# Kernel tuning notes

Hardware: AMD Instinct MI355X
Metric: run time of the kernel (lower is better)

The kernel has to match this reference:

```python
import jax, jax.numpy as jnp
import numpy as np

N_REF, N_IN, D_FEAT, P, N_ELEM = 4096, 8192, 512, 256, 4


def setup_inputs() -> dict:
    key = jax.random.key(0)
    k1, k2, k3, k4, k5 = jax.random.split(key, 5)
    return {
        "Alpha": jax.random.normal(k1, (P, N_REF), dtype=jnp.float32) * 0.05,
        "X_ref": jax.random.normal(k2, (N_REF, D_FEAT), dtype=jnp.float32),
        "desc": jax.random.normal(k3, (N_IN, D_FEAT), dtype=jnp.float32),
        "Z_ref": jax.random.randint(k4, (N_REF,), 0, N_ELEM, dtype=jnp.int32),
        "Z": jax.random.randint(k5, (N_IN,), 0, N_ELEM, dtype=jnp.int32),
        "expK": 2,
    }


def reference(Alpha, X_ref, desc, Z_ref, Z, expK):
    # Per-element grouped kernel: K[i, j] = (X_ref[i] . desc[j])**expK,
    # contribution only where ref atom i and query atom j share the element.
    # This is exactly the gather -> per-element GEMM+pow -> combine -> scatter
    # of the original module, expressed as one masked dense computation.
    K = jnp.power(jnp.matmul(X_ref, desc.T), expK)          # [N_ref, N_in]
    same_elem = Z_ref[:, None] == Z[None, :]                # [N_ref, N_in]
    K_masked = jnp.where(same_elem, K, jnp.zeros((), K.dtype))
    y = jnp.matmul(Alpha, K_masked)                          # [P, N_in]
    return y
```

## Files before the change

kernel.cpp:

```cpp
#include <hip/hip_runtime.h>
#include <stdint.h>

#define P_DIM 256
#define NREF  4096
#define NIN   8192
#define DF    512
#define NE    4
#define CREF  1536
#define CIN   2560
#define AE_LD (NE * CREF)

typedef __bf16 bf16x8 __attribute__((ext_vector_type(8)));
typedef float  f32x4  __attribute__((ext_vector_type(4)));
typedef unsigned short ush8 __attribute__((ext_vector_type(8)));

static __device__ __forceinline__ unsigned short f2bf(float f) {
    uint32_t u = __builtin_bit_cast(uint32_t, f);
    u += 0x7FFFu + ((u >> 16) & 1u);
    return (unsigned short)(u >> 16);
}

__global__ __launch_bounds__(256) void plan_sort(
    const int* __restrict__ Zr, const int* __restrict__ Z,
    int* __restrict__ iperm, int* __restrict__ jperm, int* __restrict__ cnt) {
    __shared__ int histX[NE][256];
    __shared__ int histD[NE][256];
    const int t = threadIdx.x;
    constexpr int CHX = NREF / 256;
    constexpr int CHD = NIN / 256;

    int lc[NE];
#pragma unroll
    for (int e = 0; e < NE; ++e) lc[e] = 0;
    for (int k = 0; k < CHX; ++k) lc[Zr[t * CHX + k] & (NE - 1)]++;
#pragma unroll
    for (int e = 0; e < NE; ++e) histX[e][t] = lc[e];

#pragma unroll
    for (int e = 0; e < NE; ++e) lc[e] = 0;
    for (int k = 0; k < CHD; ++k) lc[Z[t * CHD + k] & (NE - 1)]++;
#pragma unroll
    for (int e = 0; e < NE; ++e) histD[e][t] = lc[e];

    __syncthreads();
    if (t < 2 * NE) {
        int b = t & (NE - 1);
        int isD = t >> 2;
        int run = 0;
        if (!isD) {
            for (int u = 0; u < 256; ++u) { int v = histX[b][u]; histX[b][u] = run; run += v; }
            cnt[b] = run;
        } else {
            for (int u = 0; u < 256; ++u) { int v = histD[b][u]; histD[b][u] = run; run += v; }
            cnt[NE + b] = run;
        }
    }
    __syncthreads();

    int off[NE];
#pragma unroll
    for (int e = 0; e < NE; ++e) off[e] = histX[e][t];
    for (int k = 0; k < CHX; ++k) {
        int i = t * CHX + k;
        int e = Zr[i] & (NE - 1);
        iperm[e * CREF + off[e]++] = i;
    }
#pragma unroll
    for (int e = 0; e < NE; ++e) off[e] = histD[e][t];
    for (int k = 0; k < CHD; ++k) {
        int j = t * CHD + k;
        int e = Z[j] & (NE - 1);
        jperm[e * CIN + off[e]++] = j;
    }
}

#define GATHER_BLOCKS (NE * (CREF + CIN) / 4)
#define ALPHA_BLOCKS  (P_DIM * AE_LD / (256 * 8))

__global__ void gather_all(const float* __restrict__ Alpha,
                           const float* __restrict__ X_ref, const float* __restrict__ desc,
                           const int* __restrict__ iperm, const int* __restrict__ jperm,
                           const int* __restrict__ cnt,
                           unsigned short* __restrict__ Xe, unsigned short* __restrict__ De,
                           unsigned short* __restrict__ Ae) {
    if (blockIdx.x < GATHER_BLOCKS) {
        int w = (blockIdx.x * blockDim.x + threadIdx.x) >> 6;
        int lane = threadIdx.x & 63;
        const float* src = nullptr;
        unsigned short* dstp;
        if (w < NE * CREF) {
            int e = w / CREF, s = w - e * CREF;
            if (s < cnt[e]) src = X_ref + (size_t)iperm[w] * DF;
            dstp = Xe + (size_t)w * DF;
        } else {
            int w2 = w - NE * CREF;
            int e = w2 / CIN, s = w2 - e * CIN;
            if (s < cnt[NE + e]) src = desc + (size_t)jperm[w2] * DF;
            dstp = De + (size_t)w2 * DF;
        }
        ush8 o;
        if (src) {
            float4 a = *(const float4*)(src + lane * 8);
            float4 b = *(const float4*)(src + lane * 8 + 4);
            o[0] = f2bf(a.x); o[1] = f2bf(a.y); o[2] = f2bf(a.z); o[3] = f2bf(a.w);
            o[4] = f2bf(b.x); o[5] = f2bf(b.y); o[6] = f2bf(b.z); o[7] = f2bf(b.w);
        } else {
            o = (ush8){0, 0, 0, 0, 0, 0, 0, 0};
        }
        *(ush8*)(dstp + lane * 8) = o;
    } else {
        int idx8 = (blockIdx.x - GATHER_BLOCKS) * 256 + threadIdx.x;
        int p = idx8 / (AE_LD / 8);
        int c8 = idx8 - p * (AE_LD / 8);
        int col0 = c8 * 8;
        int e = col0 / CREF;
        int ic0 = col0 - e * CREF;
        int cn = cnt[e];
        const int* ip = iperm + col0;
        ush8 v;
#pragma unroll
        for (int k = 0; k < 8; ++k) {
            unsigned short r = 0;
            if (ic0 + k < cn) r = f2bf(Alpha[(size_t)p * NREF + ip[k]]);
            v[k] = r;
        }
        *(ush8*)(Ae + (size_t)idx8 * 8) = v;
    }
}

__global__ __launch_bounds__(256) void g1_grouped(
    const unsigned short* __restrict__ DeA, const unsigned short* __restrict__ XeA,
    unsigned short* __restrict__ KtA, const int* __restrict__ cnt) {
    constexpr int BK = 64;
    const int e = blockIdx.z;
    const int padR = (cnt[e] + 127) & ~127;
    const int padI = (cnt[NE + e] + 127) & ~127;
    const int m0 = blockIdx.y * 128;
    const int n0 = blockIdx.x * 128;
    if (m0 >= padI || n0 >= padR) return;

    const unsigned short* A = DeA + (size_t)e * CIN * DF;
    const unsigned short* B = XeA + (size_t)e * CREF * DF;
    unsigned short* C = KtA + (size_t)e * CIN * CREF;

    __shared__ unsigned short tA[128 * BK];
    __shared__ unsigned short tB[128 * BK];

    const int tid = threadIdx.x, wave = tid >> 6, lane = tid & 63;
    const int wr = wave >> 1, wc = wave & 1;
    const int waveM = wr * 64, waveN = wc * 64;
    const int lrow = lane >> 3, ls = lane & 7;
    const int l15 = lane & 15, lq = lane >> 4;

    f32x4 acc[4][4];
#pragma unroll
    for (int r = 0; r < 4; ++r)
#pragma unroll
        for (int c = 0; c < 4; ++c) acc[r][c] = (f32x4){0.f, 0.f, 0.f, 0.f};

#pragma unroll 1
    for (int k0 = 0; k0 < DF; k0 += BK) {
        __syncthreads();
#pragma unroll
        for (int it = 0; it < 8; ++it) {
            int cb = wave + it * 4;
            bool isB = cb >= 16;
            int cb2 = isB ? cb - 16 : cb;
            int row = cb2 * 8 + lrow;
            int g = ls ^ (row & 7);
            const unsigned short* gp = (isB ? B : A)
                + (size_t)((isB ? n0 : m0) + row) * DF + (size_t)(k0 + g * 8);
            unsigned short* lp = (isB ? tB : tA) + cb2 * (8 * BK);
            __builtin_amdgcn_global_load_lds(
                (const __attribute__((address_space(1))) void*)gp,
                (__attribute__((address_space(3))) void*)lp, 16, 0, 0);
        }
        __syncthreads();
#pragma unroll
        for (int kk = 0; kk < BK; kk += 32) {
            const int cbase = kk >> 3;
            bf16x8 af[4], bfr[4];
#pragma unroll
            for (int r = 0; r < 4; ++r) {
                int m = waveM + r * 16 + l15;
                int ch = (cbase + lq) ^ (m & 7);
                af[r] = *(const bf16x8*)&tA[m * BK + ch * 8];
            }
#pragma unroll
            for (int c = 0; c < 4; ++c) {
                int n = waveN + c * 16 + l15;
                int ch = (cbase + lq) ^ (n & 7);
                bfr[c] = *(const bf16x8*)&tB[n * BK + ch * 8];
            }
#pragma unroll
            for (int r = 0; r < 4; ++r)
#pragma unroll
                for (int c = 0; c < 4; ++c)
                    acc[r][c] = __builtin_amdgcn_mfma_f32_16x16x32_bf16(
                        af[r], bfr[c], acc[r][c], 0, 0, 0);
        }
    }

#pragma unroll
    for (int r = 0; r < 4; ++r) {
        int mb = m0 + waveM + r * 16 + lq * 4;
#pragma unroll
        for (int reg = 0; reg < 4; ++reg) {
            size_t ro = (size_t)(mb + reg) * CREF;
#pragma unroll
            for (int c = 0; c < 4; ++c) {
                int n = n0 + waveN + c * 16 + l15;
                float v = acc[r][c][reg];
                C[ro + n] = f2bf(v * v);
            }
        }
    }
}

__global__ __launch_bounds__(256) void g2_grouped(
    const unsigned short* __restrict__ Ae, const unsigned short* __restrict__ KtA,
    const int* __restrict__ jperm, const int* __restrict__ cnt,
    float* __restrict__ out) {
    constexpr int BK = 64;
    const int e = blockIdx.z;
    const int cntI = cnt[NE + e];
    const int padR = (cnt[e] + 127) & ~127;
    const int n0 = blockIdx.x * 64;
    const int m0 = blockIdx.y * 128;
    if (n0 >= cntI) return;

    const unsigned short* B = KtA + (size_t)e * CIN * CREF;

    __shared__ unsigned short tA[2][128 * BK];
    __shared__ unsigned short tB[2][64 * BK];

    const int tid = threadIdx.x, wave = tid >> 6, lane = tid & 63;
    const int wr = wave >> 1, wc = wave & 1;
    const int waveM = wr * 64, waveN = wc * 32;
    const int lrow = lane >> 3, ls = lane & 7;
    const int l15 = lane & 15, lq = lane >> 4;

    auto stage = [&](int buf, int k0) {
#pragma unroll
        for (int it = 0; it < 6; ++it) {
            int cb = wave + it * 4;
            bool isB = cb >= 16;
            int cb2 = isB ? cb - 16 : cb;
            int row = cb2 * 8 + lrow;
            int g = ls ^ (row & 7);
            const unsigned short* gp = isB
                ? B + (size_t)(n0 + row) * CREF + (size_t)(k0 + g * 8)
                : Ae + (size_t)(m0 + row) * AE_LD + (size_t)(e * CREF + k0 + g * 8);
            unsigned short* lp = (isB ? tB[buf] : tA[buf]) + cb2 * (8 * BK);
            __builtin_amdgcn_global_load_lds(
                (const __attribute__((address_space(1))) void*)gp,
                (__attribute__((address_space(3))) void*)lp, 16, 0, 0);
        }
    };

    f32x4 acc[4][2];
#pragma unroll
    for (int r = 0; r < 4; ++r)
#pragma unroll
        for (int c = 0; c < 2; ++c) acc[r][c] = (f32x4){0.f, 0.f, 0.f, 0.f};

    if (padR > 0) {
        stage(0, 0);
        __syncthreads();
        int buf = 0;
#pragma unroll 1
        for (int k0 = 0; k0 < padR; k0 += BK) {
            if (k0 + BK < padR) stage(buf ^ 1, k0 + BK);
#pragma unroll
            for (int kk = 0; kk < BK; kk += 32) {
                const int cbase = kk >> 3;
                bf16x8 af[4], bfr[2];
#pragma unroll
                for (int r = 0; r < 4; ++r) {
                    int m = waveM + r * 16 + l15;
                    int ch = (cbase + lq) ^ (m & 7);
                    af[r] = *(const bf16x8*)&tA[buf][m * BK + ch * 8];
                }
#pragma unroll
                for (int c = 0; c < 2; ++c) {
                    int n = waveN + c * 16 + l15;
                    int ch = (cbase + lq) ^ (n & 7);
                    bfr[c] = *(const bf16x8*)&tB[buf][n * BK + ch * 8];
                }
#pragma unroll
                for (int r = 0; r < 4; ++r)
#pragma unroll
                    for (int c = 0; c < 2; ++c)
                        acc[r][c] = __builtin_amdgcn_mfma_f32_16x16x32_bf16(
                            af[r], bfr[c], acc[r][c], 0, 0, 0);
            }
            __syncthreads();
            buf ^= 1;
        }
    }

    int jok[2], jdest[2];
#pragma unroll
    for (int c = 0; c < 2; ++c) {
        int jl = n0 + waveN + c * 16 + l15;
        jok[c] = jl < cntI;
        jdest[c] = jok[c] ? jperm[e * CIN + jl] : 0;
    }
#pragma unroll
    for (int r = 0; r < 4; ++r) {
        int pb = m0 + waveM + r * 16 + lq * 4;
#pragma unroll
        for (int reg = 0; reg < 4; ++reg) {
            size_t ro = (size_t)(pb + reg) * NIN;
#pragma unroll
            for (int c = 0; c < 2; ++c)
                if (jok[c]) out[ro + jdest[c]] = acc[r][c][reg];
        }
    }
}

extern "C" void kernel_launch(void* const* d_in, const int* in_sizes, int n_in,
                              void* d_out, int out_size, void* d_ws, size_t ws_size,
                              hipStream_t stream) {
    const float* Alpha = (const float*)d_in[0];
    const float* X_ref = (const float*)d_in[1];
    const float* desc  = (const float*)d_in[2];
    const int*   Z_ref = (const int*)d_in[3];
    const int*   Z     = (const int*)d_in[4];
    float* out = (float*)d_out;

    unsigned short* Xe = (unsigned short*)d_ws;
    unsigned short* De = Xe + (size_t)NE * CREF * DF;
    unsigned short* Ae = De + (size_t)NE * CIN * DF;
    unsigned short* Kt = Ae + (size_t)P_DIM * AE_LD;
    int* iperm = (int*)(Kt + (size_t)NE * CIN * CREF);
    int* jperm = iperm + NE * CREF;
    int* cnt   = jperm + NE * CIN;

    plan_sort<<<1, 256, 0, stream>>>(Z_ref, Z, iperm, jperm, cnt);

    gather_all<<<GATHER_BLOCKS + ALPHA_BLOCKS, 256, 0, stream>>>(
        Alpha, X_ref, desc, iperm, jperm, cnt, Xe, De, Ae);

    g1_grouped<<<dim3(CREF / 128, CIN / 128, NE), 256, 0, stream>>>(De, Xe, Kt, cnt);

    g2_grouped<<<dim3(CIN / 64, P_DIM / 128, NE), 256, 0, stream>>>(Ae, Kt, jperm, cnt, out);
}
```

Baseline: 150.9 us.

## Fuse gather and both grouped GEMMs into one persistent kernel with grid barriers

After: 387.8 us. +156.9%, slower.

```diff
diff --git a/kernel.cpp b/kernel.cpp
--- a/kernel.cpp
+++ b/kernel.cpp
@@ -9,6 +9,7 @@
 #define CREF  1536
 #define CIN   2560
 #define AE_LD (NE * CREF)
+#define NBLK  512
 
 typedef __bf16 bf16x8 __attribute__((ext_vector_type(8)));
 typedef float  f32x4  __attribute__((ext_vector_type(4)));
@@ -20,14 +21,28 @@
     return (unsigned short)(u >> 16);
 }
 
+static __device__ __forceinline__ void gridbar(int* b) {
+    __syncthreads();
+    if (threadIdx.x == 0) {
+        __threadfence();
+        __hip_atomic_fetch_add(b, 1, __ATOMIC_ACQ_REL, __HIP_MEMORY_SCOPE_AGENT);
+        while (__hip_atomic_load(b, __ATOMIC_ACQUIRE, __HIP_MEMORY_SCOPE_AGENT) < NBLK)
+            __builtin_amdgcn_s_sleep(2);
+    }
+    __syncthreads();
+}
+
 __global__ __launch_bounds__(256) void plan_sort(
     const int* __restrict__ Zr, const int* __restrict__ Z,
-    int* __restrict__ iperm, int* __restrict__ jperm, int* __restrict__ cnt) {
+    int* __restrict__ iperm, int* __restrict__ jperm, int* __restrict__ cnt,
+    int* __restrict__ bar) {
     __shared__ int histX[NE][256];
     __shared__ int histD[NE][256];
     const int t = threadIdx.x;
     constexpr int CHX = NREF / 256;
     constexpr int CHD = NIN / 256;
+
+    if (t < 2) bar[t] = 0;
 
     int lc[NE];
 #pragma unroll
@@ -77,244 +92,252 @@
 #define GATHER_BLOCKS (NE * (CREF + CIN) / 4)
 #define ALPHA_BLOCKS  (P_DIM * AE_LD / (256 * 8))
 
-__global__ void gather_all(const float* __restrict__ Alpha,
-                           const float* __restrict__ X_ref, const float* __restrict__ desc,
-                           const int* __restrict__ iperm, const int* __restrict__ jperm,
-                           const int* __restrict__ cnt,
-                           unsigned short* __restrict__ Xe, unsigned short* __restrict__ De,
-                           unsigned short* __restrict__ Ae) {
-    if (blockIdx.x < GATHER_BLOCKS) {
-        int w = (blockIdx.x * blockDim.x + threadIdx.x) >> 6;
-        int lane = threadIdx.x & 63;
-        const float* src = nullptr;
-        unsigned short* dstp;
-        if (w < NE * CREF) {
-            int e = w / CREF, s = w - e * CREF;
-            if (s < cnt[e]) src = X_ref + (size_t)iperm[w] * DF;
-            dstp = Xe + (size_t)w * DF;
-        } else {
-            int w2 = w - NE * CREF;
-            int e = w2 / CIN, s = w2 - e * CIN;
-            if (s < cnt[NE + e]) src = desc + (size_t)jperm[w2] * DF;
-            dstp = De + (size_t)w2 * DF;
-        }
-        ush8 o;
-        if (src) {
-            float4 a = *(const float4*)(src + lane * 8);
-            float4 b = *(const float4*)(src + lane * 8 + 4);
-            o[0] = f2bf(a.x); o[1] = f2bf(a.y); o[2] = f2bf(a.z); o[3] = f2bf(a.w);
-            o[4] = f2bf(b.x); o[5] = f2bf(b.y); o[6] = f2bf(b.z); o[7] = f2bf(b.w);
-        } else {
-            o = (ush8){0, 0, 0, 0, 0, 0, 0, 0};
-        }
-        *(ush8*)(dstp + lane * 8) = o;
-    } else {
-        int idx8 = (blockIdx.x - GATHER_BLOCKS) * 256 + threadIdx.x;
-        int p = idx8 / (AE_LD / 8);
-        int c8 = idx8 - p * (AE_LD / 8);
-        int col0 = c8 * 8;
-        int e = col0 / CREF;
-        int ic0 = col0 - e * CREF;
-        int cn = cnt[e];
-        const int* ip = iperm + col0;
-        ush8 v;
-#pragma unroll
-        for (int k = 0; k < 8; ++k) {
-            unsigned short r = 0;
-            if (ic0 + k < cn) r = f2bf(Alpha[(size_t)p * NREF + ip[k]]);
-            v[k] = r;
-        }
-        *(ush8*)(Ae + (size_t)idx8 * 8) = v;
-    }
-}
-
-__global__ __launch_bounds__(256) void g1_grouped(
-    const unsigned short* __restrict__ DeA, const unsigned short* __restrict__ XeA,
-    unsigned short* __restrict__ KtA, const int* __restrict__ cnt) {
+__global__ __launch_bounds__(256, 2) void fused_all(
+    const float* __restrict__ Alpha, const float* __restrict__ X_ref,
+    const float* __restrict__ desc,
+    const int* __restrict__ iperm, const int* __restrict__ jperm,
+    const int* __restrict__ cnt,
+    unsigned short* __restrict__ Xe, unsigned short* __restrict__ De,
+    unsigned short* __restrict__ Ae, unsigned short* __restrict__ KtA,
+    float* __restrict__ out, int* __restrict__ bar) {
     constexpr int BK = 64;
-    const int e = blockIdx.z;
-    const int padR = (cnt[e] + 127) & ~127;
-    const int padI = (cnt[NE + e] + 127) & ~127;
-    const int m0 = blockIdx.y * 128;
-    const int n0 = blockIdx.x * 128;
-    if (m0 >= padI || n0 >= padR) return;
-
-    const unsigned short* A = DeA + (size_t)e * CIN * DF;
-    const unsigned short* B = XeA + (size_t)e * CREF * DF;
-    unsigned short* C = KtA + (size_t)e * CIN * CREF;
-
-    __shared__ unsigned short tA[128 * BK];
-    __shared__ unsigned short tB[128 * BK];
+    __shared__ unsigned short lds[24576];
 
     const int tid = threadIdx.x, wave = tid >> 6, lane = tid & 63;
     const int wr = wave >> 1, wc = wave & 1;
-    const int waveM = wr * 64, waveN = wc * 64;
     const int lrow = lane >> 3, ls = lane & 7;
     const int l15 = lane & 15, lq = lane >> 4;
 
-    f32x4 acc[4][4];
-#pragma unroll
-    for (int r = 0; r < 4; ++r)
-#pragma unroll
-        for (int c = 0; c < 4; ++c) acc[r][c] = (f32x4){0.f, 0.f, 0.f, 0.f};
-
-#pragma unroll 1
-    for (int k0 = 0; k0 < DF; k0 += BK) {
-        __syncthreads();
-#pragma unroll
-        for (int it = 0; it < 8; ++it) {
-            int cb = wave + it * 4;
-            bool isB = cb >= 16;
-            int cb2 = isB ? cb - 16 : cb;
-            int row = cb2 * 8 + lrow;
-            int g = ls ^ (row & 7);
-            const unsigned short* gp = (isB ? B : A)
-                + (size_t)((isB ? n0 : m0) + row) * DF + (size_t)(k0 + g * 8);
-            unsigned short* lp = (isB ? tB : tA) + cb2 * (8 * BK);
-            __builtin_amdgcn_global_load_lds(
-                (const __attribute__((address_space(1))) void*)gp,
-                (__attribute__((address_space(3))) void*)lp, 16, 0, 0);
+#pragma unroll 1
+    for (int vb = blockIdx.x; vb < GATHER_BLOCKS + ALPHA_BLOCKS; vb += NBLK) {
+        if (vb < GATHER_BLOCKS) {
+            int w = (vb * 256 + tid) >> 6;
+            const float* src = nullptr;
+            unsigned short* dstp;
+            if (w < NE * CREF) {
+                int e = w / CREF, s = w - e * CREF;
+                if (s < cnt[e]) src = X_ref + (size_t)iperm[w] * DF;
+                dstp = Xe + (size_t)w * DF;
+            } else {
+                int w2 = w - NE * CREF;
+                int e = w2 / CIN, s = w2 - e * CIN;
+                if (s < cnt[NE + e]) src = desc + (size_t)jperm[w2] * DF;
+                dstp = De + (size_t)w2 * DF;
+            }
+            ush8 o;
+            if (src) {
+                float4 a = *(const float4*)(src + lane * 8);
+                float4 b = *(const float4*)(src + lane * 8 + 4);
+                o[0] = f2bf(a.x); o[1] = f2bf(a.y); o[2] = f2bf(a.z); o[3] = f2bf(a.w);
+                o[4] = f2bf(b.x); o[5] = f2bf(b.y); o[6] = f2bf(b.z); o[7] = f2bf(b.w);
+            } else {
+                o = (ush8){0, 0, 0, 0, 0, 0, 0, 0};
+            }
+            *(ush8*)(dstp + lane * 8) = o;
+        } else {
+            int idx8 = (vb - GATHER_BLOCKS) * 256 + tid;
+            int p = idx8 / (AE_LD / 8);
+            int c8 = idx8 - p * (AE_LD / 8);
+            int col0 = c8 * 8;
+            int e = col0 / CREF;
+            int ic0 = col0 - e * CREF;
+            int cn = cnt[e];
+            const int* ip = iperm + col0;
+            ush8 v;
+#pragma unroll
+            for (int k = 0; k < 8; ++k) {
+                unsigned short r = 0;
+                if (ic0 + k < cn) r = f2bf(Alpha[(size_t)p * NREF + ip[k]]);
+                v[k] = r;
+            }
+            *(ush8*)(Ae + (size_t)idx8 * 8) = v;
         }
-        __syncthreads();
-#pragma unroll
-        for (int kk = 0; kk < BK; kk += 32) {
-            const int cbase = kk >> 3;
-            bf16x8 af[4], bfr[4];
+    }
+
+    gridbar(bar + 0);
+
+    {
+        unsigned short* tA = lds;
+        unsigned short* tB = lds + 8192;
+#pragma unroll 1
+        for (int vt = blockIdx.x; vt < (CREF / 128) * (CIN / 128) * NE; vt += NBLK) {
+            const int bx = vt % (CREF / 128);
+            const int rem = vt / (CREF / 128);
+            const int by = rem % (CIN / 128);
+            const int e = rem / (CIN / 128);
+            const int padR = (cnt[e] + 127) & ~127;
+            const int padI = (cnt[NE + e] + 127) & ~127;
+            const int m0 = by * 128;
+            const int n0 = bx * 128;
+            if (m0 >= padI || n0 >= padR) continue;
+
+            const unsigned short* A = De + (size_t)e * CIN * DF;
+            const unsigned short* B = Xe + (size_t)e * CREF * DF;
+            unsigned short* C = KtA + (size_t)e * CIN * CREF;
+
+            f32x4 acc[4][4];
+#pragma unroll
+            for (int r = 0; r < 4; ++r)
+#pragma unroll
+                for (int c = 0; c < 4; ++c) acc[r][c] = (f32x4){0.f, 0.f, 0.f, 0.f};
+
+            const int waveM = wr * 64, waveN = wc * 64;
+#pragma unroll 1
+            for (int k0 = 0; k0 < DF; k0 += BK) {
+                __syncthreads();
+#pragma unroll
+                for (int it = 0; it < 8; ++it) {
+                    int cb = wave + it * 4;
+                    bool isB = cb >= 16;
+                    int cb2 = isB ? cb - 16 : cb;
+                    int row = cb2 * 8 + lrow;
+                    int g = ls ^ (row & 7);
+                    const unsigned short* gp = (isB ? B : A)
+                        + (size_t)((isB ? n0 : m0) + row) * DF + (size_t)(k0 + g * 8);
+                    unsigned short* lp = (isB ? tB : tA) + cb2 * (8 * BK);
+                    __builtin_amdgcn_global_load_lds(
+                        (const __attribute__((address_space(1))) void*)gp,
+                        (__attribute__((address_space(3))) void*)lp, 16, 0, 0);
+                }
+                __syncthreads();
+#pragma unroll
+                for (int kk = 0; kk < BK; kk += 32) {
+                    const int cbase = kk >> 3;
+                    bf16x8 af[4], bfr[4];
+#pragma unroll
+                    for (int r = 0; r < 4; ++r) {
+                        int m = waveM + r * 16 + l15;
+                        int ch = (cbase + lq) ^ (m & 7);
+                        af[r] = *(const bf16x8*)&tA[m * BK + ch * 8];
+                    }
+#pragma unroll
+                    for (int c = 0; c < 4; ++c) {
+                        int n = waveN + c * 16 + l15;
+                        int ch = (cbase + lq) ^ (n & 7);
+                        bfr[c] = *(const bf16x8*)&tB[n * BK + ch * 8];
+                    }
+#pragma unroll
+                    for (int r = 0; r < 4; ++r)
+#pragma unroll
+                        for (int c = 0; c < 4; ++c)
+                            acc[r][c] = __builtin_amdgcn_mfma_f32_16x16x32_bf16(
+                                af[r], bfr[c], acc[r][c], 0, 0, 0);
+                }
+            }
+
 #pragma unroll
             for (int r = 0; r < 4; ++r) {
-                int m = waveM + r * 16 + l15;
-                int ch = (cbase + lq) ^ (m & 7);
-                af[r] = *(const bf16x8*)&tA[m * BK + ch * 8];
-            }
-#pragma unroll
-            for (int c = 0; c < 4; ++c) {
-                int n = waveN + c * 16 + l15;
-                int ch = (cbase + lq) ^ (n & 7);
-                bfr[c] = *(const bf16x8*)&tB[n * BK + ch * 8];
-            }
+                int mb = m0 + waveM + r * 16 + lq * 4;
+#pragma unroll
+                for (int reg = 0; reg < 4; ++reg) {
+                    size_t ro = (size_t)(mb + reg) * CREF;
+#pragma unroll
+                    for (int c = 0; c < 4; ++c) {
+                        int n = n0 + waveN + c * 16 + l15;
+                        float v = acc[r][c][reg];
+                        C[ro + n] = f2bf(v * v);
+                    }
+                }
+            }
+        }
+    }
+
+    gridbar(bar + 1);
+
+    {
+        unsigned short* tA2 = lds;
+        unsigned short* tB2 = lds + 16384;
+#pragma unroll 1
+        for (int vt = blockIdx.x; vt < (CIN / 64) * (P_DIM / 128) * NE; vt += NBLK) {
+            const int bx = vt % (CIN / 64);
+            const int rem = vt / (CIN / 64);
+            const int by = rem % (P_DIM / 128);
+            const int e = rem / (P_DIM / 128);
+            const int cntI = cnt[NE + e];
+            const int padR = (cnt[e] + 127) & ~127;
+            const int n0 = bx * 64;
+            const int m0 = by * 128;
+            if (n0 >= cntI) continue;
+
+            const unsigned short* B = KtA + (size_t)e * CIN * CREF;
+            const int waveM = wr * 64, waveN = wc * 32;
+
+            auto stage = [&](int buf, int k0) {
+#pragma unroll
+                for (int it = 0; it < 6; ++it) {
+                    int cb = wave + it * 4;
+                    bool isB = cb >= 16;
+                    int cb2 = isB ? cb - 16 : cb;
+                    int row = cb2 * 8 + lrow;
+                    int g = ls ^ (row & 7);
+                    const unsigned short* gp = isB
+                        ? B + (size_t)(n0 + row) * CREF + (size_t)(k0 + g * 8)
+                        : Ae + (size_t)(m0 + row) * AE_LD + (size_t)(e * CREF + k0 + g * 8);
+                    unsigned short* lp = (isB ? tB2 + buf * 4096 : tA2 + buf * 8192)
+                        + cb2 * (8 * BK);
+                    __builtin_amdgcn_global_load_lds(
+                        (const __attribute__((address_space(1))) void*)gp,
+                        (__attribute__((address_space(3))) void*)lp, 16, 0, 0);
+                }
+            };
+
+            f32x4 acc[4][2];
 #pragma unroll
             for (int r = 0; r < 4; ++r)
 #pragma unroll
-                for (int c = 0; c < 4; ++c)
-                    acc[r][c] = __builtin_amdgcn_mfma_f32_16x16x32_bf16(
-                        af[r], bfr[c], acc[r][c], 0, 0, 0);
-        }
-    }
-
-#pragma unroll
-    for (int r = 0; r < 4; ++r) {
-        int mb = m0 + waveM + r * 16 + lq * 4;
-#pragma unroll
-        for (int reg = 0; reg < 4; ++reg) {
-            size_t ro = (size_t)(mb + reg) * CREF;
-#pragma unroll
-            for (int c = 0; c < 4; ++c) {
-                int n = n0 + waveN + c * 16 + l15;
-                float v = acc[r][c][reg];
-                C[ro + n] = f2bf(v * v);
-            }
-        }
-    }
-}
-
-__global__ __launch_bounds__(256) void g2_grouped(
-    const unsigned short* __restrict__ Ae, const unsigned short* __restrict__ KtA,
-    const int* __restrict__ jperm, const int* __restrict__ cnt,
-    float* __restrict__ out) {
-    constexpr int BK = 64;
-    const int e = blockIdx.z;
-    const int cntI = cnt[NE + e];
-    const int padR = (cnt[e] + 127) & ~127;
-    const int n0 = blockIdx.x * 64;
-    const int m0 = blockIdx.y * 128;
-    if (n0 >= cntI) return;
-
-    const unsigned short* B = KtA + (size_t)e * CIN * CREF;
-
-    __shared__ unsigned short tA[2][128 * BK];
-    __shared__ unsigned short tB[2][64 * BK];
-
-    const int tid = threadIdx.x, wave = tid >> 6, lane = tid & 63;
-    const int wr = wave >> 1, wc = wave & 1;
-    const int waveM = wr * 64, waveN = wc * 32;
-    const int lrow = lane >> 3, ls = lane & 7;
-    const int l15 = lane & 15, lq = lane >> 4;
-
-    auto stage = [&](int buf, int k0) {
-#pragma unroll
-        for (int it = 0; it < 6; ++it) {
-            int cb = wave + it * 4;
-            bool isB = cb >= 16;
-            int cb2 = isB ? cb - 16 : cb;
-            int row = cb2 * 8 + lrow;
-            int g = ls ^ (row & 7);
-            const unsigned short* gp = isB
-                ? B + (size_t)(n0 + row) * CREF + (size_t)(k0 + g * 8)
-                : Ae + (size_t)(m0 + row) * AE_LD + (size_t)(e * CREF + k0 + g * 8);
-            unsigned short* lp = (isB ? tB[buf] : tA[buf]) + cb2 * (8 * BK);
-            __builtin_amdgcn_global_load_lds(
-                (const __attribute__((address_space(1))) void*)gp,
-                (__attribute__((address_space(3))) void*)lp, 16, 0, 0);
-        }
-    };
-
-    f32x4 acc[4][2];
-#pragma unroll
-    for (int r = 0; r < 4; ++r)
-#pragma unroll
-        for (int c = 0; c < 2; ++c) acc[r][c] = (f32x4){0.f, 0.f, 0.f, 0.f};
-
-    if (padR > 0) {
-        stage(0, 0);
-        __syncthreads();
-        int buf = 0;
-#pragma unroll 1
-        for (int k0 = 0; k0 < padR; k0 += BK) {
-            if (k0 + BK < padR) stage(buf ^ 1, k0 + BK);
-#pragma unroll
-            for (int kk = 0; kk < BK; kk += 32) {
-                const int cbase = kk >> 3;
-                bf16x8 af[4], bfr[2];
-#pragma unroll
-                for (int r = 0; r < 4; ++r) {
-                    int m = waveM + r * 16 + l15;
-                    int ch = (cbase + lq) ^ (m & 7);
-                    af[r] = *(const bf16x8*)&tA[buf][m * BK + ch * 8];
-                }
-#pragma unroll
-                for (int c = 0; c < 2; ++c) {
-                    int n = waveN + c * 16 + l15;
-                    int ch = (cbase + lq) ^ (n & 7);
-                    bfr[c] = *(const bf16x8*)&tB[buf][n * BK + ch * 8];
-                }
-#pragma unroll
-                for (int r = 0; r < 4; ++r)
+                for (int c = 0; c < 2; ++c) acc[r][c] = (f32x4){0.f, 0.f, 0.f, 0.f};
+
+            stage(0, 0);
+            __syncthreads();
+            int buf = 0;
+#pragma unroll 1
+            for (int k0 = 0; k0 < padR; k0 += BK) {
+                if (k0 + BK < padR) stage(buf ^ 1, k0 + BK);
+#pragma unroll
+                for (int kk = 0; kk < BK; kk += 32) {
+                    const int cbase = kk >> 3;
+                    bf16x8 af[4], bfr[2];
+#pragma unroll
+                    for (int r = 0; r < 4; ++r) {
+                        int m = waveM + r * 16 + l15;
+                        int ch = (cbase + lq) ^ (m & 7);
+                        af[r] = *(const bf16x8*)&tA2[buf * 8192 + m * BK + ch * 8];
+                    }
+#pragma unroll
+                    for (int c = 0; c < 2; ++c) {
+                        int n = waveN + c * 16 + l15;
+                        int ch = (cbase + lq) ^ (n & 7);
+                        bfr[c] = *(const bf16x8*)&tB2[buf * 4096 + n * BK + ch * 8];
+                    }
+#pragma unroll
+                    for (int r = 0; r < 4; ++r)
+#pragma unroll
+                        for (int c = 0; c < 2; ++c)
+                            acc[r][c] = __builtin_amdgcn_mfma_f32_16x16x32_bf16(
+                                af[r], bfr[c], acc[r][c], 0, 0, 0);
+                }
+                __syncthreads();
+                buf ^= 1;
+            }
+
+            int jok[2], jdest[2];
+#pragma unroll
+            for (int c = 0; c < 2; ++c) {
+                int jl = n0 + waveN + c * 16 + l15;
+                jok[c] = jl < cntI;
+                jdest[c] = jok[c] ? jperm[e * CIN + jl] : 0;
+            }
+#pragma unroll
+            for (int r = 0; r < 4; ++r) {
+                int pb = m0 + waveM + r * 16 + lq * 4;
+#pragma unroll
+                for (int reg = 0; reg < 4; ++reg) {
+                    size_t ro = (size_t)(pb + reg) * NIN;
 #pragma unroll
                     for (int c = 0; c < 2; ++c)
-                        acc[r][c] = __builtin_amdgcn_mfma_f32_16x16x32_bf16(
-                            af[r], bfr[c], acc[r][c], 0, 0, 0);
-            }
-            __syncthreads();
-            buf ^= 1;
-        }
-    }
-
-    int jok[2], jdest[2];
-#pragma unroll
-    for (int c = 0; c < 2; ++c) {
-        int jl = n0 + waveN + c * 16 + l15;
-        jok[c] = jl < cntI;
-        jdest[c] = jok[c] ? jperm[e * CIN + jl] : 0;
-    }
-#pragma unroll
-    for (int r = 0; r < 4; ++r) {
-        int pb = m0 + waveM + r * 16 + lq * 4;
-#pragma unroll
-        for (int reg = 0; reg < 4; ++reg) {
-            size_t ro = (size_t)(pb + reg) * NIN;
-#pragma unroll
-            for (int c = 0; c < 2; ++c)
-                if (jok[c]) out[ro + jdest[c]] = acc[r][c][reg];
+                        if (jok[c]) out[ro + jdest[c]] = acc[r][c][reg];
+                }
+            }
         }
     }
 }
@@ -336,13 +359,10 @@
     int* iperm = (int*)(Kt + (size_t)NE * CIN * CREF);
     int* jperm = iperm + NE * CREF;
     int* cnt   = jperm + NE * CIN;
-
-    plan_sort<<<1, 256, 0, stream>>>(Z_ref, Z, iperm, jperm, cnt);
-
-    gather_all<<<GATHER_BLOCKS + ALPHA_BLOCKS, 256, 0, stream>>>(
-        Alpha, X_ref, desc, iperm, jperm, cnt, Xe, De, Ae);
-
-    g1_grouped<<<dim3(CREF / 128, CIN / 128, NE), 256, 0, stream>>>(De, Xe, Kt, cnt);
-
-    g2_grouped<<<dim3(CIN / 64, P_DIM / 128, NE), 256, 0, stream>>>(Ae, Kt, jperm, cnt, out);
-}
+    int* bar   = cnt + 8;
+
+    plan_sort<<<1, 256, 0, stream>>>(Z_ref, Z, iperm, jperm, cnt, bar);
+
+    fused_all<<<NBLK, 256, 0, stream>>>(Alpha, X_ref, desc, iperm, jperm, cnt,
+                                        Xe, De, Ae, Kt, out, bar);
+}
```
